# Optimization experiments

Hardware: AMD Instinct MI355X
Metric: run time of the kernel (lower is better)

Reference implementation:

```python
import jax, jax.numpy as jnp
import numpy as np

H = 1024
V = 32000
L = 15
B = 512


def setup_inputs() -> dict:
    key = jax.random.key(0)
    ks = jax.random.split(key, 16)
    s = 0.02
    return {
        "input_ids": jax.random.randint(ks[0], (B,), 0, V),
        "hidden": jax.random.normal(ks[1], (1, B, H), jnp.float32),
        "encoder_outputs": jax.random.normal(ks[2], (L, B, H), jnp.float32),
        "max_length": L,
        "embedding": jax.random.normal(ks[3], (V, H), jnp.float32) * s,
        "attn1_w": jax.random.normal(ks[4], (1, 2 * H), jnp.float32) * s,
        "attn1_b": jnp.zeros((1,), jnp.float32),
        "combine_w": jax.random.normal(ks[5], (H, 2 * H), jnp.float32) * s,
        "combine_b": jnp.zeros((H,), jnp.float32),
        "w_ih": jax.random.normal(ks[6], (3 * H, H), jnp.float32) * s,
        "w_hh": jax.random.normal(ks[7], (3 * H, H), jnp.float32) * s,
        "b_ih": jnp.zeros((3 * H,), jnp.float32),
        "b_hh": jnp.zeros((3 * H,), jnp.float32),
        "out_w": jax.random.normal(ks[8], (V, H), jnp.float32) * s,
        "out_b": jnp.zeros((V,), jnp.float32),
    }


def reference(input_ids, hidden, encoder_outputs, max_length, embedding,
              attn1_w, attn1_b, combine_w, combine_b,
              w_ih, w_hh, b_ih, b_hh, out_w, out_b):
    # embedding lookup (dropout is identity in eval mode)
    emb = embedding[input_ids]                       # [B, H]
    # Bahdanau-style additive scores: vectorize the per-step python loop
    emb_l = jnp.broadcast_to(emb[None], (max_length, B, H))   # [L, B, H]
    cat = jnp.concatenate([emb_l, encoder_outputs], axis=-1)  # [L, B, 2H]
    scores = cat @ attn1_w.T + attn1_b               # [L, B, 1]
    attn_weights = jax.nn.softmax(scores, axis=0)    # softmax over L
    ctx = jnp.sum(attn_weights * encoder_outputs, axis=0)     # [B, H]
    x = jnp.concatenate([emb, ctx], axis=-1) @ combine_w.T + combine_b  # [B, H]
    # n_layers = 1: relu then one GRU step (seq len 1)
    x = jax.nn.relu(x)
    h = hidden[0]                                    # [B, H]
    gi = x @ w_ih.T + b_ih                           # [B, 3H]
    gh = h @ w_hh.T + b_hh                           # [B, 3H]
    i_r, i_z, i_n = jnp.split(gi, 3, axis=1)
    h_r, h_z, h_n = jnp.split(gh, 3, axis=1)
    r = jax.nn.sigmoid(i_r + h_r)
    z = jax.nn.sigmoid(i_z + h_z)
    n = jnp.tanh(i_n + r * h_n)
    h_new = (1.0 - z) * n + z * h                    # [B, H]
    logits = h_new @ out_w.T + out_b                 # [B, V]
    output = jax.nn.log_softmax(logits, axis=1)
    return output, h_new[None], attn_weights
```

## Files before the change

kernel.cpp:

```cpp
#include <hip/hip_runtime.h>

#define HH 1024
#define VV 32000
#define LL 15
#define BB 512

typedef __bf16 bf16;
typedef __bf16 bf16x4 __attribute__((ext_vector_type(4)));
typedef __bf16 bf16x8 __attribute__((ext_vector_type(8)));
typedef float f32x4 __attribute__((ext_vector_type(4)));

#define VMCNT(n) asm volatile("s_waitcnt vmcnt(" #n ")" ::: "memory")
#define SBAR     __builtin_amdgcn_s_barrier()
#define SCHED0   __builtin_amdgcn_sched_barrier(0)

__device__ __forceinline__ unsigned short f2bf(float f) {
    unsigned int u = __float_as_uint(f);
    unsigned int r = (u + 0x7fffu + ((u >> 16) & 1u)) >> 16;
    return (unsigned short)r;
}
__device__ __forceinline__ float bf2f(unsigned short u) {
    return __uint_as_float(((unsigned int)u) << 16);
}

__device__ __forceinline__ void gld_lds16(const void* g, void* l) {
    __builtin_amdgcn_global_load_lds(
        (const __attribute__((address_space(1))) unsigned int*)g,
        (__attribute__((address_space(3))) unsigned int*)l, 16, 0, 0);
}

#define PACKU  (VV * HH / 8)
#define CVT0   (3 * HH * HH / 8)
#define CVT1   (3 * HH * HH / 8)
#define CVT2   (2 * HH * HH / 8)
#define CVT3   (BB * HH / 8)
#define NPACKB 2000
#define NCVTB  544

__global__ __launch_bounds__(256)
void stream_kernel(const float* __restrict__ out_w, unsigned short* __restrict__ packed,
                   const float* __restrict__ w_ih, unsigned short* __restrict__ w_ih_bf,
                   const float* __restrict__ w_hh, unsigned short* __restrict__ w_hh_bf,
                   const float* __restrict__ combine_w, unsigned short* __restrict__ w_cb_bf,
                   const float* __restrict__ hidden, unsigned short* __restrict__ hid_bf) {
    const int bid = blockIdx.x, tid = threadIdx.x;
    f32x4 a[8], b[8];

    if (bid < NPACKB) {
        const int u0 = bid * 2048 + tid;
        #pragma unroll
        for (int q = 0; q < 8; q++) {
            const int u = u0 + q * 256;
            const int g = u >> 14, dd = u & 16383;
            const int kt = dd >> 10, ot = dd & 1023;
            const float* src = out_w + ((size_t)((g << 7) + (ot >> 3))) * 1024
                               + (kt << 6) + ((ot & 7) << 3);
            a[q] = *(const f32x4*)src;
            b[q] = *(const f32x4*)(src + 4);
        }
        #pragma unroll
        for (int q = 0; q < 8; q++) {
            const bf16x4 wa = __builtin_convertvector(a[q], bf16x4);
            const bf16x4 wb = __builtin_convertvector(b[q], bf16x4);
            bf16x8 w;
            #pragma unroll
            for (int c = 0; c < 4; c++) { w[c] = wa[c]; w[c + 4] = wb[c]; }
            *(bf16x8*)&packed[(size_t)(u0 + q * 256) * 8] = w;
        }
        return;
    }

    int ub = (bid - NPACKB) * 2048 + tid;
    const float* src; unsigned short* dst;
    if (ub < CVT0) { src = w_ih; dst = w_ih_bf; }
    else if ((ub -= CVT0) < CVT1) { src = w_hh; dst = w_hh_bf; }
    else if ((ub -= CVT1) < CVT2) { src = combine_w; dst = w_cb_bf; }
    else { ub -= CVT2; src = hidden; dst = hid_bf; }

    #pragma unroll
    for (int q = 0; q < 8; q++) {
        const int i = ub + q * 256;
        a[q] = ((const f32x4*)src)[2 * i];
        b[q] = ((const f32x4*)src)[2 * i + 1];
    }
    #pragma unroll
    for (int q = 0; q < 8; q++) {
        const int i = ub + q * 256;
        const bf16x4 wa = __builtin_convertvector(a[q], bf16x4);
        const bf16x4 wb = __builtin_convertvector(b[q], bf16x4);
        bf16x8 w;
        #pragma unroll
        for (int c = 0; c < 4; c++) { w[c] = wa[c]; w[c + 4] = wb[c]; }
        *(bf16x8*)&dst[(size_t)i * 8] = w;
    }
}

__global__ __launch_bounds__(256)
void attn_kernel(const int* __restrict__ ids, const float* __restrict__ enc,
                 const float* __restrict__ embedding,
                 const float* __restrict__ attn1_w, const float* __restrict__ attn1_b,
                 float* __restrict__ attn_out, unsigned short* __restrict__ cat_out) {
    const int b = blockIdx.x, tid = threadIdx.x;
    const int lane = tid & 63, wv = tid >> 6;

    __shared__ float s_enc[LL * HH];
    __shared__ float s_scores[LL];
    __shared__ float s_red[4];

    for (int idx = tid; idx < LL * HH / 4; idx += 256) {
        const int l = (idx * 4) >> 10, h = (idx * 4) & (HH - 1);
        *(f32x4*)&s_enc[idx * 4] = *(const f32x4*)&enc[((size_t)l * BB + b) * HH + h];
    }

    const float* embr = embedding + (size_t)ids[b] * HH;
    float p = 0.f;
    for (int j = tid; j < HH; j += 256) p += embr[j] * attn1_w[j];
    #pragma unroll
    for (int o = 32; o; o >>= 1) p += __shfl_xor(p, o);
    if (lane == 0) s_red[wv] = p;
    __syncthreads();
    const float semb = s_red[0] + s_red[1] + s_red[2] + s_red[3] + attn1_b[0];

    for (int l = wv; l < LL; l += 4) {
        float q = 0.f;
        for (int j = lane; j < HH; j += 64) q += s_enc[l * HH + j] * attn1_w[HH + j];
        #pragma unroll
        for (int o = 32; o; o >>= 1) q += __shfl_xor(q, o);
        if (lane == 0) s_scores[l] = q + semb;
    }
    __syncthreads();

    float mx = -3.4e38f;
    #pragma unroll
    for (int l = 0; l < LL; l++) mx = fmaxf(mx, s_scores[l]);
    float aw[LL], sum = 0.f;
    #pragma unroll
    for (int l = 0; l < LL; l++) { aw[l] = __expf(s_scores[l] - mx); sum += aw[l]; }
    const float inv = 1.f / sum;
    #pragma unroll
    for (int l = 0; l < LL; l++) aw[l] *= inv;

    if (tid < LL) attn_out[tid * BB + b] = aw[tid];

    for (int j = tid; j < HH; j += 256) {
        float c = 0.f;
        #pragma unroll
        for (int l = 0; l < LL; l++) c += aw[l] * s_enc[l * HH + j];
        cat_out[(size_t)b * (2 * HH) + j] = f2bf(embr[j]);
        cat_out[(size_t)b * (2 * HH) + HH + j] = f2bf(c);
    }
}

template<int TM, int TN, int OUT, int GATES>
__global__ __launch_bounds__(256)
void gemm_nt(const bf16* __restrict__ A, const bf16* __restrict__ B,
             const float* __restrict__ bias, void* __restrict__ Cout,
             const bf16* __restrict__ A2, const bf16* __restrict__ B2,
             const float* __restrict__ bias2, void* __restrict__ C2,
             const int K, const int N) {
    constexpr int FM = TM / 32, FN = TN / 32;
    __shared__ bf16 As[2][TM * 64];
    __shared__ bf16 Bs[2][TN * 64];

    if (GATES && blockIdx.z == 1) { A = A2; B = B2; bias = bias2; Cout = C2; }

    const int tid = threadIdx.x;
    const int lane = tid & 63, wave = tid >> 6;
    const int wm = wave >> 1, wn = wave & 1;
    const int rlo = lane & 15, khi = lane >> 4;
    const int m0 = blockIdx.y * TM, n0 = blockIdx.x * TN;

    f32x4 acc[FM][FN] = {};
    constexpr int IA = TM / 32, IB = TN / 32;

    auto stage = [&](int k0, int buf) {
        #pragma unroll
        for (int i = 0; i < IA; i++) {
            const int p = (i * 256 + tid) * 16;
            const int row = p >> 7;
            const int qs = (p & 127) ^ ((row & 7) << 4);
            gld_lds16(A + (size_t)(m0 + row) * K + k0 + (qs >> 1),
                      &As[buf][0] + i * 2048 + wave * 512);
        }
        #pragma unroll
        for (int i = 0; i < IB; i++) {
            const int p = (i * 256 + tid) * 16;
            const int row = p >> 7;
            const int qs = (p & 127) ^ ((row & 7) << 4);
            gld_lds16(B + (size_t)(n0 + row) * K + k0 + (qs >> 1),
                      &Bs[buf][0] + i * 2048 + wave * 512);
        }
    };

    auto compute = [&](int buf) {
        #pragma unroll
        for (int ks = 0; ks < 2; ks++) {
            bf16x8 af[FM], bfr[FN];
            #pragma unroll
            for (int m = 0; m < FM; m++) {
                const int r = wm * (TM / 2) + m * 16 + rlo;
                const int sw = (ks * 64 + khi * 16) ^ ((r & 7) << 4);
                af[m] = *(const bf16x8*)((const char*)&As[buf][0] + r * 128 + sw);
            }
            #pragma unroll
            for (int n = 0; n < FN; n++) {
                const int r = wn * (TN / 2) + n * 16 + rlo;
                const int sw = (ks * 64 + khi * 16) ^ ((r & 7) << 4);
                bfr[n] = *(const bf16x8*)((const char*)&Bs[buf][0] + r * 128 + sw);
            }
            #pragma unroll
            for (int m = 0; m < FM; m++)
                #pragma unroll
                for (int n = 0; n < FN; n++)
                    acc[m][n] = __builtin_amdgcn_mfma_f32_16x16x32_bf16(af[m], bfr[n], acc[m][n], 0, 0, 0);
        }
    };

    const int NT = K >> 6;
    stage(0, 0);
    stage(64, 1);

    for (int kt = 0; kt < NT; kt += 2) {
        {
            const int t = kt;
            if (t + 1 < NT) { VMCNT(4); } else { VMCNT(0); }
            SCHED0; SBAR; SCHED0;
            compute(0);
            SCHED0; SBAR; SCHED0;
            if (t + 2 < NT) stage((t + 2) << 6, 0);
        }
        {
            const int t = kt + 1;
            if (t + 1 < NT) { VMCNT(4); } else { VMCNT(0); }
            SCHED0; SBAR; SCHED0;
            compute(1);
            SCHED0; SBAR; SCHED0;
            if (t + 2 < NT) stage((t + 2) << 6, 1);
        }
    }

    #pragma unroll
    for (int m = 0; m < FM; m++) {
        const int gr = m0 + wm * (TM / 2) + m * 16 + khi * 4;
        #pragma unroll
        for (int n = 0; n < FN; n++) {
            const int gc = n0 + wn * (TN / 2) + n * 16 + rlo;
            const float bv = bias[gc];
            #pragma unroll
            for (int j = 0; j < 4; j++) {
                float v = acc[m][n][j] + bv;
                if (OUT == 1) {
                    v = fmaxf(v, 0.f);
                    ((unsigned short*)Cout)[(size_t)(gr + j) * N + gc] = f2bf(v);
                } else {
                    ((float*)Cout)[(size_t)(gr + j) * N + gc] = v;
                }
            }
        }
    }
}

template<int CB>
__global__ __launch_bounds__(256, 2)
void gemm_out(const bf16* __restrict__ A, const bf16* __restrict__ Bp,
              const float* __restrict__ bias, float* __restrict__ C,
              unsigned short* __restrict__ Cb,
              float* __restrict__ pmax, float* __restrict__ psum) {
    constexpr int K = HH, N = VV;
    __shared__ bf16 As[2][128 * 64];
    __shared__ bf16 Bs[2][128 * 64];
    __shared__ float sPm[2][128], sPs[2][128];

    const int tid = threadIdx.x;
    const int lane = tid & 63, wave = tid >> 6;
    const int wm = wave >> 1, wn = wave & 1;
    const int rlo = lane & 15, khi = lane >> 4;

    constexpr int gridN = 250;
    constexpr int nFull = (gridN >> 3) << 5;
    const int bidx = blockIdx.x;
    int g, jm;
    if (bidx < nFull) { const int s = bidx >> 5, rem = bidx & 31; jm = rem >> 3; g = s * 8 + (rem & 7); }
    else { const int rem = bidx - nFull; constexpr int gleft = gridN & 7; g = (gridN & ~7) + rem % gleft; jm = rem / gleft; }
    const int n0 = g * 128, m0 = jm * 128;

    const char* pb = (const char*)(Bp + (size_t)g * 131072);

    f32x4 acc[4][4] = {};

    auto stage = [&](int k0, int buf) {
        #pragma unroll
        for (int i = 0; i < 4; i++) {
            const int p = (i * 256 + tid) * 16;
            const int row = p >> 7;
            const int qs = (p & 127) ^ ((row & 7) << 4);
            gld_lds16(A + (size_t)(m0 + row) * K + k0 + (qs >> 1),
                      &As[buf][0] + i * 2048 + wave * 512);
        }
        #pragma unroll
        for (int i = 0; i < 4; i++) {
            const int p = (i * 256 + tid) * 16;
            const int row = p >> 7;
            const int qs = (p & 127) ^ ((row & 7) << 4);
            gld_lds16(pb + (size_t)(k0 >> 6) * 16384 + row * 128 + qs,
                      &Bs[buf][0] + i * 2048 + wave * 512);
        }
    };

    auto compute = [&](int buf) {
        #pragma unroll
        for (int ks = 0; ks < 2; ks++) {
            bf16x8 af[4], bfr[4];
            #pragma unroll
            for (int m = 0; m < 4; m++) {
                const int r = wm * 64 + m * 16 + rlo;
                const int sw = (ks * 64 + khi * 16) ^ ((r & 7) << 4);
                af[m] = *(const bf16x8*)((const char*)&As[buf][0] + r * 128 + sw);
            }
            #pragma unroll
            for (int n = 0; n < 4; n++) {
                const int r = wn * 64 + n * 16 + rlo;
                const int sw = (ks * 64 + khi * 16) ^ ((r & 7) << 4);
                bfr[n] = *(const bf16x8*)((const char*)&Bs[buf][0] + r * 128 + sw);
            }
            #pragma unroll
            for (int m = 0; m < 4; m++)
                #pragma unroll
                for (int n = 0; n < 4; n++)
                    acc[m][n] = __builtin_amdgcn_mfma_f32_16x16x32_bf16(af[m], bfr[n], acc[m][n], 0, 0, 0);
        }
    };

    constexpr int NT = K >> 6;
    stage(0, 0);
    stage(64, 1);

    for (int kt = 0; kt < NT; kt += 2) {
        {
            const int t = kt;
            if (t + 1 < NT) { VMCNT(8); } else { VMCNT(0); }
            SCHED0; SBAR; SCHED0;
            compute(0);
            SCHED0; SBAR; SCHED0;
            if (t + 2 < NT) stage((t + 2) << 6, 0);
        }
        {
            const int t = kt + 1;
            if (t + 1 < NT) { VMCNT(8); } else { VMCNT(0); }
            SCHED0; SBAR; SCHED0;
            compute(1);
            SCHED0; SBAR; SCHED0;
            if (t + 2 < NT) stage((t + 2) << 6, 1);
        }
    }

    float bvn[4];
    #pragma unroll
    for (int n = 0; n < 4; n++) bvn[n] = bias[n0 + wn * 64 + n * 16 + rlo];

    #pragma unroll
    for (int m = 0; m < 4; m++) {
        const int rbase = wm * 64 + m * 16 + khi * 4;
        #pragma unroll
        for (int j = 0; j < 4; j++) {
            const int gr = m0 + rbase + j;
            float v[4];
            float lm = -3.4e38f;
            #pragma unroll
            for (int n = 0; n < 4; n++) {
                v[n] = acc[m][n][j] + bvn[n];
                const size_t ci = (size_t)gr * N + n0 + wn * 64 + n * 16 + rlo;
                if (CB) Cb[ci] = f2bf(v[n]); else C[ci] = v[n];
                lm = fmaxf(lm, v[n]);
            }
            #pragma unroll
            for (int o = 8; o; o >>= 1) lm = fmaxf(lm, __shfl_xor(lm, o));
            float ls = 0.f;
            #pragma unroll
            for (int n = 0; n < 4; n++) ls += __expf(v[n] - lm);
            #pragma unroll
            for (int o = 8; o; o >>= 1) ls += __shfl_xor(ls, o);
            if (rlo == 0) { sPm[wn][rbase + j] = lm; sPs[wn][rbase + j] = ls; }
        }
    }
    __syncthreads();
    if (tid < 128) {
        const float ma = sPm[0][tid], mb = sPm[1][tid];
        const float M = fmaxf(ma, mb);
        const float S = sPs[0][tid] * __expf(ma - M) + sPs[1][tid] * __expf(mb - M);
        pmax[(size_t)(m0 + tid) * 256 + g] = M;
        psum[(size_t)(m0 + tid) * 256 + g] = S;
    }
}

__global__ __launch_bounds__(256)
void gru_kernel(const float* __restrict__ gi, const float* __restrict__ gh,
                const float* __restrict__ h, float* __restrict__ hnew,
                unsigned short* __restrict__ hnew_bf) {
    const int i = blockIdx.x * 256 + threadIdx.x;
    const int e = i * 4;
    const int b = e >> 10, j = e & (HH - 1);
    const size_t o = ((size_t)b * 3 * HH + j) / 4;
    const f32x4 ir = ((const f32x4*)gi)[o],          iz = ((const f32x4*)gi)[o + HH / 4],
                in_ = ((const f32x4*)gi)[o + 2 * HH / 4];
    const f32x4 hr = ((const f32x4*)gh)[o],          hz = ((const f32x4*)gh)[o + HH / 4],
                hn = ((const f32x4*)gh)[o + 2 * HH / 4];
    const f32x4 hv = ((const f32x4*)h)[i];
    f32x4 out;
    ushort4 ob;
    #pragma unroll
    for (int c = 0; c < 4; c++) {
        const float r = 1.f / (1.f + __expf(-(ir[c] + hr[c])));
        const float z = 1.f / (1.f + __expf(-(iz[c] + hz[c])));
        const float n = tanhf(in_[c] + r * hn[c]);
        const float v = (1.f - z) * n + z * hv[c];
        out[c] = v;
        ((unsigned short*)&ob)[c] = f2bf(v);
    }
    ((f32x4*)hnew)[i] = out;
    ((ushort4*)hnew_bf)[i] = ob;
}

template<int CB>
__global__ __launch_bounds__(512)
void lsm_final(const float* __restrict__ pmax, const float* __restrict__ psum,
               const unsigned short* __restrict__ Cb, float* __restrict__ logits) {
    const int b = blockIdx.x, tid = threadIdx.x;
    const int lane = tid & 63, wv = tid >> 6;
    __shared__ float sm[8], ss[8];

    float m = -3.4e38f, s = 0.f;
    if (tid < 250) { m = pmax[(size_t)b * 256 + tid]; s = psum[(size_t)b * 256 + tid]; }
    #pragma unroll
    for (int o = 32; o; o >>= 1) {
        const float mo = __shfl_xor(m, o), so = __shfl_xor(s, o);
        const float nm = fmaxf(m, mo);
        s = s * __expf(m - nm) + so * __expf(mo - nm);
        m = nm;
    }
    if (lane == 0) { sm[wv] = m; ss[wv] = s; }
    __syncthreads();
    float M = sm[0], S;
    #pragma unroll
    for (int w = 1; w < 8; w++) M = fmaxf(M, sm[w]);
    S = ss[0] * __expf(sm[0] - M);
    #pragma unroll
    for (int w = 1; w < 8; w++) S += ss[w] * __expf(sm[w] - M);
    const float lse = M + __logf(S);

    float* row = logits + (size_t)b * VV;
    if (CB) {
        const unsigned short* rowc = Cb + (size_t)b * VV;
        for (int j = tid; j < VV / 8; j += 512) {
            const ushort4 u0 = ((const ushort4*)rowc)[2 * j];
            const ushort4 u1 = ((const ushort4*)rowc)[2 * j + 1];
            f32x4 v0, v1;
            v0[0] = bf2f(u0.x) - lse; v0[1] = bf2f(u0.y) - lse;
            v0[2] = bf2f(u0.z) - lse; v0[3] = bf2f(u0.w) - lse;
            v1[0] = bf2f(u1.x) - lse; v1[1] = bf2f(u1.y) - lse;
            v1[2] = bf2f(u1.z) - lse; v1[3] = bf2f(u1.w) - lse;
            ((f32x4*)row)[2 * j] = v0;
            ((f32x4*)row)[2 * j + 1] = v1;
        }
    } else {
        for (int j = tid; j < VV / 4; j += 512) {
            f32x4 v = ((const f32x4*)row)[j];
            v[0] -= lse; v[1] -= lse; v[2] -= lse; v[3] -= lse;
            ((f32x4*)row)[j] = v;
        }
    }
}

extern "C" void kernel_launch(void* const* d_in, const int* in_sizes, int n_in,
                              void* d_out, int out_size, void* d_ws, size_t ws_size,
                              hipStream_t stream) {
    const int*   ids       = (const int*)d_in[0];
    const float* hidden    = (const float*)d_in[1];
    const float* enc       = (const float*)d_in[2];
    const float* embedding = (const float*)d_in[4];
    const float* attn1_w   = (const float*)d_in[5];
    const float* attn1_b   = (const float*)d_in[6];
    const float* combine_w = (const float*)d_in[7];
    const float* combine_b = (const float*)d_in[8];
    const float* w_ih      = (const float*)d_in[9];
    const float* w_hh      = (const float*)d_in[10];
    const float* b_ih      = (const float*)d_in[11];
    const float* b_hh      = (const float*)d_in[12];
    const float* out_w     = (const float*)d_in[13];
    const float* out_b     = (const float*)d_in[14];

    float* out_lsm = (float*)d_out;
    float* out_h   = out_lsm + (size_t)BB * VV;
    float* out_aw  = out_h + (size_t)BB * HH;

    char* w = (char*)d_ws;
    unsigned short* packed   = (unsigned short*)w;   w += (size_t)VV * HH * 2;
    unsigned short* w_ih_bf  = (unsigned short*)w;   w += (size_t)3 * HH * HH * 2;
    unsigned short* w_hh_bf  = (unsigned short*)w;   w += (size_t)3 * HH * HH * 2;
    unsigned short* w_cb_bf  = (unsigned short*)w;   w += (size_t)2 * HH * HH * 2;
    unsigned short* cat_bf   = (unsigned short*)w;   w += (size_t)BB * 2 * HH * 2;
    unsigned short* x_bf     = (unsigned short*)w;   w += (size_t)BB * HH * 2;
    unsigned short* hid_bf   = (unsigned short*)w;   w += (size_t)BB * HH * 2;
    unsigned short* hnew_bf  = (unsigned short*)w;   w += (size_t)BB * HH * 2;
    float* gi   = (float*)w;                         w += (size_t)BB * 3 * HH * 4;
    float* gh   = (float*)w;                         w += (size_t)BB * 3 * HH * 4;
    float* pmax = (float*)w;                         w += (size_t)BB * 256 * 4;
    float* psum = (float*)w;                         w += (size_t)BB * 256 * 4;
    unsigned short* Cb = (unsigned short*)w;
    const size_t needed_cb = (size_t)(w - (char*)d_ws) + (size_t)BB * VV * 2;
    const bool use_cb = ws_size >= needed_cb;

    stream_kernel<<<NPACKB + NCVTB, 256, 0, stream>>>(
        out_w, packed, w_ih, w_ih_bf, w_hh, w_hh_bf, combine_w, w_cb_bf, hidden, hid_bf);

    attn_kernel<<<BB, 256, 0, stream>>>(ids, enc, embedding, attn1_w, attn1_b, out_aw, cat_bf);

    gemm_nt<64, 64, 1, 0><<<dim3(HH / 64, BB / 64), 256, 0, stream>>>(
        (const bf16*)cat_bf, (const bf16*)w_cb_bf, combine_b, x_bf,
        nullptr, nullptr, nullptr, nullptr, 2 * HH, HH);

    gemm_nt<64, 64, 0, 1><<<dim3(3 * HH / 64, BB / 64, 2), 256, 0, stream>>>(
        (const bf16*)hid_bf, (const bf16*)w_hh_bf, b_hh, gh,
        (const bf16*)x_bf, (const bf16*)w_ih_bf, b_ih, gi, HH, 3 * HH);

    gru_kernel<<<(BB * HH / 4) / 256, 256, 0, stream>>>(gi, gh, hidden, out_h, hnew_bf);

    if (use_cb) {
        gemm_out<1><<<1000, 256, 0, stream>>>(
            (const bf16*)hnew_bf, (const bf16*)packed, out_b, nullptr, Cb, pmax, psum);
        lsm_final<1><<<BB, 512, 0, stream>>>(pmax, psum, Cb, out_lsm);
    } else {
        gemm_out<0><<<1000, 256, 0, stream>>>(
            (const bf16*)hnew_bf, (const bf16*)packed, out_b, out_lsm, nullptr, pmax, psum);
        lsm_final<0><<<BB, 512, 0, stream>>>(pmax, psum, nullptr, out_lsm);
    }
}
```

Before: 177.7 us.

## Stage out_w repack through LDS with double-buffered async global loads

The out_w fp32-to-bf16 repack blocks now read contiguous row segments with global_load_lds into a double-buffered 32KB shared buffer, then convert from LDS and write packed bf16 tiles. Coalesced loads replace the previous strided per-thread gathers, and the next chunk's fetch overlaps conversion of the current one. The generic convert path also fuses its load and convert loops, which lowers register pressure but may reduce memory-level parallelism. The extra LDS use limits occupancy, and the hand-placed vmcnt waits must exactly match the outstanding load count.

```diff
diff --git a/kernel.cpp b/kernel.cpp
--- a/kernel.cpp
+++ b/kernel.cpp
@@ -29,11 +29,9 @@
         (__attribute__((address_space(3))) unsigned int*)l, 16, 0, 0);
 }
 
-#define PACKU  (VV * HH / 8)
 #define CVT0   (3 * HH * HH / 8)
 #define CVT1   (3 * HH * HH / 8)
 #define CVT2   (2 * HH * HH / 8)
-#define CVT3   (BB * HH / 8)
 #define NPACKB 2000
 #define NCVTB  544
 
@@ -43,30 +41,56 @@
                    const float* __restrict__ w_hh, unsigned short* __restrict__ w_hh_bf,
                    const float* __restrict__ combine_w, unsigned short* __restrict__ w_cb_bf,
                    const float* __restrict__ hidden, unsigned short* __restrict__ hid_bf) {
+    __shared__ __align__(16) char smem[32768];
     const int bid = blockIdx.x, tid = threadIdx.x;
-    f32x4 a[8], b[8];
 
     if (bid < NPACKB) {
-        const int u0 = bid * 2048 + tid;
-        #pragma unroll
-        for (int q = 0; q < 8; q++) {
-            const int u = u0 + q * 256;
-            const int g = u >> 14, dd = u & 16383;
-            const int kt = dd >> 10, ot = dd & 1023;
-            const float* src = out_w + ((size_t)((g << 7) + (ot >> 3))) * 1024
-                               + (kt << 6) + ((ot & 7) << 3);
-            a[q] = *(const f32x4*)src;
-            b[q] = *(const f32x4*)(src + 4);
-        }
-        #pragma unroll
-        for (int q = 0; q < 8; q++) {
-            const bf16x4 wa = __builtin_convertvector(a[q], bf16x4);
-            const bf16x4 wb = __builtin_convertvector(b[q], bf16x4);
-            bf16x8 w;
-            #pragma unroll
-            for (int c = 0; c < 4; c++) { w[c] = wa[c]; w[c + 4] = wb[c]; }
-            *(bf16x8*)&packed[(size_t)(u0 + q * 256) * 8] = w;
-        }
+        const int g = bid >> 3;
+        const int kt0 = (bid & 7) * 2;
+        const int wave = tid >> 6;
+
+        auto stageC = [&](int c, int buf) {
+            const int kt = kt0 + (c >> 1), rh = (c & 1) * 64;
+            #pragma unroll
+            for (int i = 0; i < 4; i++) {
+                const int u = i * 256 + tid;
+                const int row = u >> 4, c16 = u & 15;
+                gld_lds16(out_w + ((size_t)(g * 128 + rh + row)) * 1024 + kt * 64 + c16 * 4,
+                          smem + buf * 16384 + i * 4096 + wave * 1024);
+            }
+        };
+        auto convC = [&](int c, int buf) {
+            const int kt = kt0 + (c >> 1), rh = (c & 1) * 64;
+            const float* sf = (const float*)(smem + buf * 16384);
+            unsigned short* dst = packed + ((size_t)(g * 16 + kt) * 128 + rh) * 64;
+            #pragma unroll
+            for (int j = 0; j < 2; j++) {
+                const int v = j * 256 + tid;
+                const f32x4 a = *(const f32x4*)(sf + v * 8);
+                const f32x4 b = *(const f32x4*)(sf + v * 8 + 4);
+                const bf16x4 wa = __builtin_convertvector(a, bf16x4);
+                const bf16x4 wb = __builtin_convertvector(b, bf16x4);
+                bf16x8 w;
+                #pragma unroll
+                for (int cc = 0; cc < 4; cc++) { w[cc] = wa[cc]; w[cc + 4] = wb[cc]; }
+                *(bf16x8*)&dst[(size_t)v * 8] = w;
+            }
+        };
+
+        stageC(0, 0); stageC(1, 1);
+        VMCNT(4); SCHED0; SBAR; SCHED0;
+        convC(0, 0);
+        SCHED0; SBAR; SCHED0;
+        stageC(2, 0);
+        VMCNT(6); SCHED0; SBAR; SCHED0;
+        convC(1, 1);
+        SCHED0; SBAR; SCHED0;
+        stageC(3, 1);
+        VMCNT(6); SCHED0; SBAR; SCHED0;
+        convC(2, 0);
+        SCHED0; SBAR; SCHED0;
+        VMCNT(2); SCHED0; SBAR; SCHED0;
+        convC(3, 1);
         return;
     }
 
@@ -80,14 +104,10 @@
     #pragma unroll
     for (int q = 0; q < 8; q++) {
         const int i = ub + q * 256;
-        a[q] = ((const f32x4*)src)[2 * i];
-        b[q] = ((const f32x4*)src)[2 * i + 1];
-    }
-    #pragma unroll
-    for (int q = 0; q < 8; q++) {
-        const int i = ub + q * 256;
-        const bf16x4 wa = __builtin_convertvector(a[q], bf16x4);
-        const bf16x4 wb = __builtin_convertvector(b[q], bf16x4);
+        const f32x4 a = ((const f32x4*)src)[2 * i];
+        const f32x4 b = ((const f32x4*)src)[2 * i + 1];
+        const bf16x4 wa = __builtin_convertvector(a, bf16x4);
+        const bf16x4 wb = __builtin_convertvector(b, bf16x4);
         bf16x8 w;
         #pragma unroll
         for (int c = 0; c < 4; c++) { w[c] = wa[c]; w[c + 4] = wb[c]; }
```

Result: no change. 179.1 us (+0.8%).
